# Kernel tuning notes

Hardware: AMD Instinct MI355X
Metric: run time of the kernel (lower is better)

Reference implementation:

```python
import jax, jax.numpy as jnp
import numpy as np

NUM_CAT = 16
SEG_LENS = np.array([4, 2, 2, 4, 4, 3, 3, 2, 4, 6, 2, 6, 3, 3, 3, 3], dtype=np.int64)
SHIFTS = np.concatenate([[0], np.cumsum(SEG_LENS)[:-1]]).astype(np.int64)
MAX_SEG_COUNT = int(SEG_LENS.max())           # 6
MAX_SEG = int(SHIFTS[-1] + SEG_LENS[-1] - 1)  # 53
IN = 128
N = 65536
EPS = 1e-5  # BatchNorm1d default eps
SLOPE = 0.2  # LeakyReLU negative slope


def setup_inputs() -> dict:
    key = jax.random.key(0)
    ks = jax.random.split(key, 4)
    features = jax.random.normal(ks[0], (N, IN), dtype=jnp.float32)
    category_labels = jax.random.randint(ks[1], (N,), 0, NUM_CAT, dtype=jnp.int64)
    # channel raising MLP: Linear(IN -> NUM_CAT*IN, bias=False)
    W1 = jax.random.normal(ks[2], (IN, NUM_CAT * IN), dtype=jnp.float32) * (1.0 / np.sqrt(IN))
    gamma = jnp.ones((NUM_CAT * IN,), dtype=jnp.float32)
    beta = jnp.zeros((NUM_CAT * IN,), dtype=jnp.float32)
    # UnaryConv weight: xavier_normal over (NUM_CAT, IN, MAX_SEG_COUNT)
    W2 = jax.random.normal(ks[3], (NUM_CAT, IN, MAX_SEG_COUNT), dtype=jnp.float32) * np.sqrt(2.0 / (IN + MAX_SEG_COUNT))
    bias = jnp.zeros((MAX_SEG_COUNT,), dtype=jnp.float32)
    return dict(features=features, W1=W1, gamma=gamma, beta=beta, W2=W2, bias=bias,
                category_labels=category_labels)


def reference(features, W1, gamma, beta, W2, bias, category_labels):
    n = features.shape[0]
    # channel raising: Linear -> BatchNorm1d (batch stats) -> LeakyReLU(0.2)
    h = features @ W1                                   # [N, C*D]
    mean = h.mean(axis=0)
    var = h.var(axis=0)                                 # biased, as in torch BN
    h = (h - mean) / jnp.sqrt(var + EPS) * gamma + beta
    h = jnp.where(h >= 0, h, SLOPE * h)
    # per-category batched matmul classifier
    h = h.reshape(n, NUM_CAT, IN).transpose(1, 0, 2)    # [C, N, D]
    logits_all = jnp.einsum('cnd,cds->cns', h, W2) + bias  # [C, N, S]
    n_idx = jnp.arange(n)
    logits = logits_all[category_labels, n_idx]         # gather: [N, S]
    logsm = jax.nn.log_softmax(logits, axis=-1)
    # scatter into per-category segment ranges of the [N, MAX_SEG+1] output
    shifts = jnp.asarray(SHIFTS)[category_labels]       # [N]
    seg_len = jnp.asarray(SEG_LENS)[category_labels]    # [N]
    s_idx = jnp.arange(MAX_SEG_COUNT)
    valid = s_idx[None, :] < seg_len[:, None]           # [N, S]
    cols = jnp.clip(shifts[:, None] + s_idx[None, :], 0, MAX_SEG)
    vals = jnp.where(valid, logsm, 0.0)                 # invalid slots add 0
    out = jnp.zeros((n, MAX_SEG + 1), dtype=logsm.dtype)
    out = out.at[n_idx[:, None], cols].add(vals)
    return out
```

## Files before the change

kernel.cpp:

```cpp
#include <hip/hip_runtime.h>
#include <hip/hip_bf16.h>

#define NCAT 16
#define BCAT 32

typedef __attribute__((ext_vector_type(8))) short short8v;
typedef __attribute__((ext_vector_type(4))) float float4v;
typedef __attribute__((ext_vector_type(16))) float f32x16;

__constant__ int c_shift[NCAT] = {0,4,6,8,12,16,19,22,24,28,34,36,42,45,48,51};
__constant__ int c_len[NCAT]   = {4,2,2,4,4,3,3,2,4,6,2,6,3,3,3,3};


static inline __device__ unsigned pk2(float lo, float hi) {
  float2 f2; f2.x = lo; f2.y = hi;
  __hip_bfloat162 h = __float22bfloat162_rn(f2);
  unsigned u; __builtin_memcpy(&u, &h, 4);
  return u;
}
static inline __device__ float bf2f(unsigned short v) {
  unsigned u = (unsigned)v << 16;
  float f; __builtin_memcpy(&f, &u, 4);
  return f;
}

template<bool PART>
__global__ __launch_bounds__(1024) void k_stats_m(
    const float* __restrict__ F, const float* __restrict__ W1,
    const float* __restrict__ W2, const int* __restrict__ lab,
    float* __restrict__ Gdst, unsigned* __restrict__ Gp16,
    float* __restrict__ sv, float* __restrict__ svpart,
    int* __restrict__ blkcnt, unsigned short* __restrict__ Wlb,
    float* __restrict__ W2p)
{
  const int tid = threadIdx.x;
  if (blockIdx.x >= 256) {
    const int cat = (int)blockIdx.x - 256;
    for (int e = tid; e < 2048; e += 1024) {
      const int fid = e >> 6, l = e & 63;
      const int ks = fid >> 3, ct = fid & 7;
      const int kb = 32 * ks + 8 * (l >> 4);
      const int c = cat * 128 + 16 * ct + (l & 15);
      uint4 pk;
      pk.x = pk2(W1[(size_t)(kb + 0) * 2048 + c], W1[(size_t)(kb + 1) * 2048 + c]);
      pk.y = pk2(W1[(size_t)(kb + 2) * 2048 + c], W1[(size_t)(kb + 3) * 2048 + c]);
      pk.z = pk2(W1[(size_t)(kb + 4) * 2048 + c], W1[(size_t)(kb + 5) * 2048 + c]);
      pk.w = pk2(W1[(size_t)(kb + 6) * 2048 + c], W1[(size_t)(kb + 7) * 2048 + c]);
      *(uint4*)(Wlb + ((size_t)(cat * 32 + fid) * 64 + l) * 8) = pk;
    }
    if (tid < 1024) {
      const int c = tid >> 3, s = tid & 7;
      W2p[cat * 1024 + tid] = (s < 6) ? W2[cat * 768 + c * 6 + s] : 0.f;
    }
    return;
  }

  __shared__ int hl[NCAT];
  if (tid < NCAT) hl[tid] = 0;
  __syncthreads();
  const int rowbase = blockIdx.x * 256;
  if (tid < 256) atomicAdd(&hl[lab[rowbase + tid]], 1);

  const int wid = tid >> 6, lane = tid & 63;
  const int wi = wid >> 2, wj = wid & 3;
  const int i0 = wi * 32, j0 = wj * 32;
  const int lr = lane & 31, lh = lane >> 5;

  f32x16 acc;
  #pragma unroll
  for (int e = 0; e < 16; ++e) acc[e] = 0.f;
  float svacc = 0.f;

  for (int ch = 0; ch < 8; ++ch) {
    #pragma unroll
    for (int h = 0; h < 2; ++h) {
      const int rbase = rowbase + ch * 32 + 16 * h + 8 * lh;
      float fa[8], fb[8];
      #pragma unroll
      for (int j = 0; j < 8; ++j) {
        const float* rp = F + (size_t)(rbase + j) * 128;
        fa[j] = rp[i0 + lr];
        fb[j] = rp[j0 + lr];
      }
      if (wj == 0) {
        #pragma unroll
        for (int j = 0; j < 8; ++j) svacc += fa[j];
      }
      uint4 av4, bv4;
      av4.x = pk2(fa[0], fa[1]); av4.y = pk2(fa[2], fa[3]);
      av4.z = pk2(fa[4], fa[5]); av4.w = pk2(fa[6], fa[7]);
      bv4.x = pk2(fb[0], fb[1]); bv4.y = pk2(fb[2], fb[3]);
      bv4.z = pk2(fb[4], fb[5]); bv4.w = pk2(fb[6], fb[7]);
      acc = __builtin_amdgcn_mfma_f32_32x32x16_bf16(
          __builtin_bit_cast(short8v, av4), __builtin_bit_cast(short8v, bv4),
          acc, 0, 0, 0);
    }
  }

  if (wj == 0) {
    svacc += __shfl_xor(svacc, 32);
    if (lane < 32) {
      if (PART) svpart[blockIdx.x * 128 + i0 + lr] = svacc;
      else      atomicAdd(&sv[i0 + lr], svacc);
    }
  }
  __syncthreads();
  if (tid < NCAT) blkcnt[blockIdx.x * NCAT + tid] = hl[tid];

  if (PART) {
    unsigned* gp = Gp16 + (size_t)blockIdx.x * 8192;
    #pragma unroll
    for (int t = 0; t < 8; ++t) {
      const int rowe = ((2 * t) & 3) + 8 * (t >> 1) + 4 * lh;
      gp[((i0 + rowe) >> 1) * 128 + j0 + lr] = pk2(acc[2 * t], acc[2 * t + 1]);
    }
  } else {
    #pragma unroll
    for (int reg = 0; reg < 16; ++reg) {
      const int row = (reg & 3) + 8 * (reg >> 2) + 4 * lh;
      atomicAdd(&Gdst[(i0 + row) * 128 + j0 + lr], acc[reg]);
    }
  }
}

__global__ __launch_bounds__(256) void k_mid(
    const unsigned* __restrict__ Gp16, const float* __restrict__ svpart,
    const int* __restrict__ blkcnt, float* __restrict__ G,
    float* __restrict__ sv, int* __restrict__ offs,
    int* __restrict__ counts, int doRed)
{
  __shared__ int ps[16][16], ps2[16][16], tot[16], catbase[16];
  const int b = blockIdx.x, tid = threadIdx.x;
  if (b < 64) {
    if (!doRed) return;
    const int e = b * 128 + (tid >> 1);
    const int half = tid & 1;
    float lo = 0.f, hi = 0.f;
    #pragma unroll 4
    for (int p = half * 128; p < half * 128 + 128; ++p) {
      const unsigned u = Gp16[(size_t)p * 8192 + e];
      lo += bf2f((unsigned short)(u & 0xffffu));
      hi += bf2f((unsigned short)(u >> 16));
    }
    lo += __shfl_xor(lo, 1);
    hi += __shfl_xor(hi, 1);
    if (half == 0) {
      const int pr = e >> 7, col = e & 127;
      G[(2 * pr) * 128 + col]     = lo;
      G[(2 * pr + 1) * 128 + col] = hi;
    }
  } else if (b == 64) {
    if (!doRed) return;
    if (tid < 128) {
      float s = 0.f;
      #pragma unroll 8
      for (int p = 0; p < 256; ++p) s += svpart[p * 128 + tid];
      sv[tid] = s;
    }
  } else {
    const int part = tid >> 4, cat = tid & 15;
    int v[16]; int s = 0;
    #pragma unroll
    for (int i = 0; i < 16; ++i) { v[i] = s; s += blkcnt[(part * 16 + i) * 16 + cat]; }
    ps[part][cat] = s;
    __syncthreads();
    if (part == 0) {
      int a = 0;
      #pragma unroll
      for (int p = 0; p < 16; ++p) { ps2[p][cat] = a; a += ps[p][cat]; }
      tot[cat] = a; counts[cat] = a;
    }
    __syncthreads();
    if (tid == 0) {
      int a = 0;
      #pragma unroll
      for (int c = 0; c < 16; ++c) { catbase[c] = a; a += tot[c]; }
    }
    __syncthreads();
    const int base = catbase[cat] + ps2[part][cat];
    #pragma unroll
    for (int i = 0; i < 16; ++i) offs[(part * 16 + i) * 16 + cat] = base + v[i];
  }
}

__global__ __launch_bounds__(256) void k_prep(
    const int* __restrict__ lab, const int* __restrict__ offs,
    const float* __restrict__ G, const float* __restrict__ sv,
    const float* __restrict__ W1, const float* __restrict__ gamma,
    const float* __restrict__ beta,
    int* __restrict__ rowidx, int* __restrict__ posidx,
    float* __restrict__ scale, float* __restrict__ shiftv)
{
  __shared__ float Gl[128][133];
  __shared__ float Wl[128][16];
  __shared__ float redq[16][16];
  __shared__ float redm[16][16];
  __shared__ int wc[4][NCAT];
  const int b = blockIdx.x, tid = threadIdx.x;
  if (b < 256) {
    const int wid = tid >> 6, lane = tid & 63;
    const int n = b * 256 + tid;
    const int c = lab[n];
    const unsigned long long lanebit = 1ull << lane;
    int myrank = 0;
    #pragma unroll
    for (int cc = 0; cc < NCAT; ++cc) {
      unsigned long long m = __ballot(c == cc);
      if (lane == 0) wc[wid][cc] = (int)__popcll(m);
      if (c == cc) myrank = (int)__popcll(m & (lanebit - 1));
    }
    __syncthreads();
    int base = 0;
    #pragma unroll
    for (int w = 0; w < 4; ++w)
      if (w < wid) base += wc[w][c];
    const int slot = offs[b * NCAT + c] + base + myrank;
    rowidx[slot] = n;
    posidx[n] = slot;
  } else {
    const int jb = (b - 256) * 16;
    for (int i = tid; i < 16384; i += 256) Gl[i >> 7][i & 127] = G[i];
    for (int i = tid; i < 2048; i += 256) {
      int k = i >> 4, col = i & 15;
      Wl[k][col] = W1[(size_t)k * 2048 + jb + col];
    }
    __syncthreads();
    const int col = tid & 15, part = tid >> 4;
    float msq = 0.f, mean = 0.f;
    for (int ii = 0; ii < 8; ++ii) {
      const int i = part * 8 + ii;
      const float wi = Wl[i][col];
      float inner = 0.f;
      #pragma unroll 8
      for (int k = 0; k < 128; ++k) inner = fmaf(Gl[i][k], Wl[k][col], inner);
      msq = fmaf(wi, inner, msq);
    }
    #pragma unroll
    for (int kk = 0; kk < 8; ++kk) {
      const int k = part * 8 + kk;
      mean = fmaf(sv[k], Wl[k][col], mean);
    }
    redq[part][col] = msq;
    redm[part][col] = mean;
    __syncthreads();
    if (tid < 16) {
      float q = 0.f, m = 0.f;
      #pragma unroll
      for (int p = 0; p < 16; ++p) { q += redq[p][tid]; m += redm[p][tid]; }
      m *= (1.f / 65536.f);
      q *= (1.f / 65536.f);
      float var = q - m * m;
      float sc = gamma[jb + tid] * rsqrtf(var + 1e-5f);
      scale[jb + tid] = sc;
      shiftv[jb + tid] = beta[jb + tid] - m * sc;
    }
  }
}

__global__ __launch_bounds__(512, 4) void k_main_g(
    const float* __restrict__ F, const unsigned short* __restrict__ Wlb,
    const float* __restrict__ W2p, const float* __restrict__ bias,
    const float* __restrict__ scale, const float* __restrict__ shiftv,
    const int* __restrict__ counts, const int* __restrict__ rowidx,
    float* __restrict__ tmp8)
{
  __shared__ __attribute__((aligned(16))) unsigned short Wl[16384];
  __shared__ __attribute__((aligned(16))) unsigned short Flds[16384];
  const int tid = threadIdx.x;
  const int cat = (int)blockIdx.x >> 5;
  const int blk = (int)blockIdx.x & (BCAT - 1);
  const int wid = tid >> 6, lane = tid & 63;
  const int lrow = lane & 15, lhi = lane >> 4;

  int off = 0, cnt = 0;
  #pragma unroll
  for (int t = 0; t < NCAT; ++t) {
    int cv = counts[t];
    if (t < cat) off += cv;
    if (t == cat) cnt = cv;
  }
  const int chunk = (cnt + BCAT - 1) / BCAT;
  const int start = off + blk * chunk;
  const int end = min(start + chunk, off + cnt);

  {
    const uint4* src = (const uint4*)(Wlb + (size_t)cat * 16384);
    uint4* dst = (uint4*)Wl;
    for (int i = tid; i < 2048; i += 512) dst[i] = src[i];
  }
  if (start >= end) return;

  float sc_r[8], sh_r[8];
  #pragma unroll
  for (int ct = 0; ct < 8; ++ct) {
    sc_r[ct] = scale[cat * 128 + ct * 16 + lrow];
    sh_r[ct] = shiftv[cat * 128 + ct * 16 + lrow];
  }
  float bi[6];
  #pragma unroll
  for (int s = 0; s < 6; ++s) bi[s] = bias[s];

  const int rsub = tid >> 5, t5 = tid & 31;

  for (int w0 = start; w0 < end; w0 += 128) {
    const int nrows = min(128, end - w0);
    __syncthreads();
    #pragma unroll
    for (int i = 0; i < 8; ++i) {
      const int rl = i * 16 + rsub;
      const int rsrc = rowidx[w0 + min(rl, nrows - 1)];
      const float4 v = *(const float4*)(F + (size_t)rsrc * 128 + t5 * 4);
      uint2 pk;
      pk.x = pk2(v.x, v.y);
      pk.y = pk2(v.z, v.w);
      *(uint2*)((char*)Flds + rl * 256 + ((t5 * 8) ^ ((rl & 7) << 4))) = pk;
    }
    __syncthreads();

    const int q0 = w0 + wid * 16;
    if (q0 < end) {
      const int lq = min(q0 + lrow, w0 + nrows - 1) - w0;
      short8v av[4];
      #pragma unroll
      for (int ks = 0; ks < 4; ++ks) {
        const int co = (ks * 64 + lhi * 16) ^ ((lq & 7) << 4);
        av[ks] = *(const short8v*)((const char*)Flds + lq * 256 + co);
      }

      float p[4][6];
      #pragma unroll
      for (int j = 0; j < 4; ++j)
        #pragma unroll
        for (int s = 0; s < 6; ++s) p[j][s] = 0.f;

      #pragma unroll
      for (int ct = 0; ct < 8; ++ct) {
        float4v acc = (float4v){0.f, 0.f, 0.f, 0.f};
        #pragma unroll
        for (int ks = 0; ks < 4; ++ks) {
          const short8v bv = *(const short8v*)(Wl + ((ks * 8 + ct) * 64 + lane) * 8);
          acc = __builtin_amdgcn_mfma_f32_16x16x32_bf16(av[ks], bv, acc, 0, 0, 0);
        }
        const int c = ct * 16 + lrow;
        const float s_ = sc_r[ct], h_ = sh_r[ct];
        const float4* w2p4 = (const float4*)(W2p + ((size_t)cat * 128 + c) * 8);
        const float4 wa = w2p4[0];
        const float4 wb4 = w2p4[1];
        const float w2v[6] = {wa.x, wa.y, wa.z, wa.w, wb4.x, wb4.y};
        #pragma unroll
        for (int j = 0; j < 4; ++j) {
          float a = acc[j] * s_ + h_;
          a = (a >= 0.f) ? a : 0.2f * a;
          #pragma unroll
          for (int s = 0; s < 6; ++s) p[j][s] = fmaf(a, w2v[s], p[j][s]);
        }
      }

      const bool b1 = (lrow & 1) != 0;
      const bool b2 = (lrow & 2) != 0;
      float q[2][6], r[6];
      #pragma unroll
      for (int t = 0; t < 2; ++t)
        #pragma unroll
        for (int s = 0; s < 6; ++s) {
          float snd = b1 ? p[2 * t][s] : p[2 * t + 1][s];
          float kp  = b1 ? p[2 * t + 1][s] : p[2 * t][s];
          q[t][s] = kp + __shfl_xor(snd, 1);
        }
      #pragma unroll
      for (int s = 0; s < 6; ++s) {
        float snd = b2 ? q[0][s] : q[1][s];
        float kp  = b2 ? q[1][s] : q[0][s];
        r[s] = kp + __shfl_xor(snd, 2);
      }
      #pragma unroll
      for (int s = 0; s < 6; ++s) r[s] += __shfl_xor(r[s], 4);
      #pragma unroll
      for (int s = 0; s < 6; ++s) r[s] += __shfl_xor(r[s], 8);

      const int jj = lrow & 3, sb = lrow >> 2;
      const int qrow = min(q0 + 4 * lhi + jj, end - 1);
      float pj[6];
      #pragma unroll
      for (int s = 0; s < 6; ++s) pj[s] = r[s] + bi[s];
      float mx = fmaxf(fmaxf(fmaxf(pj[0], pj[1]), fmaxf(pj[2], pj[3])), fmaxf(pj[4], pj[5]));
      float e = __expf(pj[0] - mx) + __expf(pj[1] - mx) + __expf(pj[2] - mx)
              + __expf(pj[3] - mx) + __expf(pj[4] - mx) + __expf(pj[5] - mx);
      float lse = mx + __logf(e);

      float4* trec = (float4*)(tmp8 + (size_t)qrow * 8);
      if (sb == 0) {
        float4 v0; v0.x = pj[0] - lse; v0.y = pj[1] - lse;
        v0.z = pj[2] - lse; v0.w = pj[3] - lse;
        trec[0] = v0;
      } else if (sb == 1) {
        float4 v1; v1.x = pj[4] - lse; v1.y = pj[5] - lse;
        v1.z = 0.f; v1.w = 0.f;
        trec[1] = v1;
      }
    }
  }
}

__global__ __launch_bounds__(256) void k_out(
    const float* __restrict__ tmp8, const int* __restrict__ lab,
    const int* __restrict__ posidx, float* __restrict__ out)
{
  const int i2 = blockIdx.x * 256 + threadIdx.x;
  const int n = i2 / 27;
  const int j2 = i2 - n * 27;
  const int c = lab[n];
  const int shc = c_shift[c], lnc = c_len[c];
  const float* rec = tmp8 + (size_t)posidx[n] * 8;
  const int s0 = 2 * j2 - shc;
  float2 v; v.x = 0.f; v.y = 0.f;
  if (s0 >= 0 && s0 < lnc)         v.x = rec[s0];
  if (s0 + 1 >= 0 && s0 + 1 < lnc) v.y = rec[s0 + 1];
  ((float2*)out)[i2] = v;
}

extern "C" void kernel_launch(void* const* d_in, const int* in_sizes, int n_in,
                              void* d_out, int out_size, void* d_ws, size_t ws_size,
                              hipStream_t stream) {
  const float* F     = (const float*)d_in[0];
  const float* W1    = (const float*)d_in[1];
  const float* gamma = (const float*)d_in[2];
  const float* beta  = (const float*)d_in[3];
  const float* W2    = (const float*)d_in[4];
  const float* bias  = (const float*)d_in[5];
  const int*   lab   = (const int*)d_in[6];
  float* out = (float*)d_out;

  char* ws = (char*)d_ws;
  float* sv      = (float*)(ws + 0);
  int*   counts  = (int*)(ws + 512);
  int*   blkcnt  = (int*)(ws + 576);
  int*   offs    = (int*)(ws + 16960);
  float* scale   = (float*)(ws + 33344);
  float* shiftv  = (float*)(ws + 41536);
  float* G       = (float*)(ws + 49728);
  int*   rowidx  = (int*)(ws + 115264);
  int*   posidx  = (int*)(ws + 377408);
  unsigned short* Wlb = (unsigned short*)(ws + 639552);
  float* W2p     = (float*)(ws + 1163840);
  float* tmp8    = (float*)(ws + 1229376);
  unsigned* Gp16 = (unsigned*)(ws + 3326528);
  float* svpart  = (float*)(ws + 11715136);

  const size_t need = 11846208;
  const int fast = (ws_size >= need) ? 1 : 0;
  if (fast) {
    hipLaunchKernelGGL(k_stats_m<true>, dim3(272), dim3(1024), 0, stream,
                       F, W1, W2, lab, G, Gp16, sv, svpart, blkcnt, Wlb, W2p);
  } else {
    hipMemsetAsync(d_ws, 0, 115264, stream);
    hipLaunchKernelGGL(k_stats_m<false>, dim3(272), dim3(1024), 0, stream,
                       F, W1, W2, lab, G, Gp16, sv, svpart, blkcnt, Wlb, W2p);
  }
  hipLaunchKernelGGL(k_mid, dim3(66), dim3(256), 0, stream,
                     Gp16, svpart, blkcnt, G, sv, offs, counts, fast);
  hipLaunchKernelGGL(k_prep, dim3(384), dim3(256), 0, stream,
                     lab, offs, G, sv, W1, gamma, beta, rowidx, posidx, scale, shiftv);
  hipLaunchKernelGGL(k_main_g, dim3(NCAT * BCAT), dim3(512), 0, stream,
                     F, Wlb, W2p, bias, scale, shiftv, counts, rowidx, tmp8);
  hipLaunchKernelGGL(k_out, dim3(6912), dim3(256), 0, stream,
                     tmp8, lab, posidx, out);
}
```

Baseline: 73.71 us.

## Split main kernel by fixed 128-row windows instead of per-category chunks

Each block in the main classifier kernel now handles one fixed 128-row window of the category-sorted rows (512 blocks covering all 65536 rows), instead of 32 blocks per category each walking a variable-length chunk. A block finds which category its window starts in and runs that segment with that category's weights. If the window crosses into the next category, it reloads the shared-memory weights and runs the remainder. This balances work evenly across blocks and removes the per-category tail imbalance. In exchange, the scale and shift values are now read from global memory inside the inner loop, and blocks that span a category boundary pay an extra weight reload and barrier. The code assumes a window never spans more than two categories.

```diff
diff --git a/kernel.cpp b/kernel.cpp
--- a/kernel.cpp
+++ b/kernel.cpp
@@ -2,7 +2,6 @@
 #include <hip/hip_bf16.h>
 
 #define NCAT 16
-#define BCAT 32
 
 typedef __attribute__((ext_vector_type(8))) short short8v;
 typedef __attribute__((ext_vector_type(4))) float float4v;
@@ -257,7 +256,7 @@
   }
 }
 
-__global__ __launch_bounds__(512, 4) void k_main_g(
+__global__ __launch_bounds__(512, 4) void k_main_w(
     const float* __restrict__ F, const unsigned short* __restrict__ Wlb,
     const float* __restrict__ W2p, const float* __restrict__ bias,
     const float* __restrict__ scale, const float* __restrict__ shiftv,
@@ -267,59 +266,50 @@
   __shared__ __attribute__((aligned(16))) unsigned short Wl[16384];
   __shared__ __attribute__((aligned(16))) unsigned short Flds[16384];
   const int tid = threadIdx.x;
-  const int cat = (int)blockIdx.x >> 5;
-  const int blk = (int)blockIdx.x & (BCAT - 1);
+  const int w0 = (int)blockIdx.x * 128;
   const int wid = tid >> 6, lane = tid & 63;
   const int lrow = lane & 15, lhi = lane >> 4;
 
-  int off = 0, cnt = 0;
-  #pragma unroll
-  for (int t = 0; t < NCAT; ++t) {
-    int cv = counts[t];
-    if (t < cat) off += cv;
-    if (t == cat) cnt = cv;
-  }
-  const int chunk = (cnt + BCAT - 1) / BCAT;
-  const int start = off + blk * chunk;
-  const int end = min(start + chunk, off + cnt);
-
+  int c0 = 0, catstart = 0;
   {
-    const uint4* src = (const uint4*)(Wlb + (size_t)cat * 16384);
-    uint4* dst = (uint4*)Wl;
-    for (int i = tid; i < 2048; i += 512) dst[i] = src[i];
-  }
-  if (start >= end) return;
-
-  float sc_r[8], sh_r[8];
-  #pragma unroll
-  for (int ct = 0; ct < 8; ++ct) {
-    sc_r[ct] = scale[cat * 128 + ct * 16 + lrow];
-    sh_r[ct] = shiftv[cat * 128 + ct * 16 + lrow];
-  }
-  float bi[6];
-  #pragma unroll
-  for (int s = 0; s < 6; ++s) bi[s] = bias[s];
-
-  const int rsub = tid >> 5, t5 = tid & 31;
-
-  for (int w0 = start; w0 < end; w0 += 128) {
-    const int nrows = min(128, end - w0);
-    __syncthreads();
+    int a = 0;
+    #pragma unroll
+    for (int t = 0; t < NCAT; ++t) {
+      const int na = a + counts[t];
+      if (w0 >= a && w0 < na) { c0 = t; catstart = a; }
+      a = na;
+    }
+  }
+  const int e0 = catstart + counts[c0];
+
+  {
+    const int rsub = tid >> 5, t5 = tid & 31;
     #pragma unroll
     for (int i = 0; i < 8; ++i) {
       const int rl = i * 16 + rsub;
-      const int rsrc = rowidx[w0 + min(rl, nrows - 1)];
+      const int rsrc = rowidx[w0 + rl];
       const float4 v = *(const float4*)(F + (size_t)rsrc * 128 + t5 * 4);
       uint2 pk;
       pk.x = pk2(v.x, v.y);
       pk.y = pk2(v.z, v.w);
       *(uint2*)((char*)Flds + rl * 256 + ((t5 * 8) ^ ((rl & 7) << 4))) = pk;
     }
-    __syncthreads();
-
-    const int q0 = w0 + wid * 16;
-    if (q0 < end) {
-      const int lq = min(q0 + lrow, w0 + nrows - 1) - w0;
+    const uint4* src = (const uint4*)(Wlb + (size_t)c0 * 16384);
+    uint4* dst = (uint4*)Wl;
+    for (int i = tid; i < 2048; i += 512) dst[i] = src[i];
+  }
+  __syncthreads();
+
+  float bi[6];
+  #pragma unroll
+  for (int s = 0; s < 6; ++s) bi[s] = bias[s];
+
+  auto do_seg = [&](int s0, int s1, int ca) {
+    const int ng = (s1 - s0 + 15) >> 4;
+    for (int g = wid; g < ng; g += 8) {
+      const int q0 = s0 + g * 16;
+      const int navail = min(16, s1 - q0);
+      const int lq = min(q0 + lrow, s1 - 1) - w0;
       short8v av[4];
       #pragma unroll
       for (int ks = 0; ks < 4; ++ks) {
@@ -342,8 +332,9 @@
           acc = __builtin_amdgcn_mfma_f32_16x16x32_bf16(av[ks], bv, acc, 0, 0, 0);
         }
         const int c = ct * 16 + lrow;
-        const float s_ = sc_r[ct], h_ = sh_r[ct];
-        const float4* w2p4 = (const float4*)(W2p + ((size_t)cat * 128 + c) * 8);
+        const float s_ = scale[ca * 128 + c];
+        const float h_ = shiftv[ca * 128 + c];
+        const float4* w2p4 = (const float4*)(W2p + ((size_t)ca * 128 + c) * 8);
         const float4 wa = w2p4[0];
         const float4 wb4 = w2p4[1];
         const float w2v[6] = {wa.x, wa.y, wa.z, wa.w, wb4.x, wb4.y};
@@ -379,7 +370,7 @@
       for (int s = 0; s < 6; ++s) r[s] += __shfl_xor(r[s], 8);
 
       const int jj = lrow & 3, sb = lrow >> 2;
-      const int qrow = min(q0 + 4 * lhi + jj, end - 1);
+      const int qrow = min(q0 + 4 * lhi + jj, s1 - 1);
       float pj[6];
       #pragma unroll
       for (int s = 0; s < 6; ++s) pj[s] = r[s] + bi[s];
@@ -398,7 +389,19 @@
         v1.z = 0.f; v1.w = 0.f;
         trec[1] = v1;
       }
-    }
+      (void)navail;
+    }
+  };
+
+  const int s1a = min(w0 + 128, e0);
+  do_seg(w0, s1a, c0);
+  if (e0 < w0 + 128) {
+    __syncthreads();
+    const uint4* src = (const uint4*)(Wlb + (size_t)(c0 + 1) * 16384);
+    uint4* dst = (uint4*)Wl;
+    for (int i = tid; i < 2048; i += 512) dst[i] = src[i];
+    __syncthreads();
+    do_seg(e0, w0 + 128, c0 + 1);
   }
 }
 
@@ -461,7 +464,7 @@
                      Gp16, svpart, blkcnt, G, sv, offs, counts, fast);
   hipLaunchKernelGGL(k_prep, dim3(384), dim3(256), 0, stream,
                      lab, offs, G, sv, W1, gamma, beta, rowidx, posidx, scale, shiftv);
-  hipLaunchKernelGGL(k_main_g, dim3(NCAT * BCAT), dim3(512), 0, stream,
+  hipLaunchKernelGGL(k_main_w, dim3(512), dim3(512), 0, stream,
                      F, Wlb, W2p, bias, scale, shiftv, counts, rowidx, tmp8);
   hipLaunchKernelGGL(k_out, dim3(6912), dim3(256), 0, stream,
                      tmp8, lab, posidx, out);
```

Result: slower. 126.0 us (+71.0%).
